# Performance work log

Hardware: AMD Instinct MI355X
Metric: run time of the kernel (lower is better)

Reference implementation:

```python
import jax, jax.numpy as jnp
import numpy as np

N_NODES = 50000
N_EDGES = 500000
N_GRAPHS = 2000
HID = 145
N_CLS = 21
N_LAYERS = 4
EPS = 1e-5

def setup_inputs() -> dict:
    key = jax.random.key(0)
    ks = jax.random.split(key, 12)
    x = jax.random.randint(ks[0], (N_NODES,), 0, N_CLS)
    edge_index = jax.random.randint(ks[1], (2, N_EDGES), 0, N_NODES)
    batch_idx = jnp.sort(jax.random.randint(ks[2], (N_NODES,), 0, N_GRAPHS))
    s = 1.0 / np.sqrt(HID)
    emb = jax.random.normal(ks[3], (N_CLS, HID), jnp.float32)
    Wc = jax.random.uniform(ks[4], (N_LAYERS, HID, HID), jnp.float32, -s, s)
    bc = jax.random.uniform(ks[5], (N_LAYERS, HID), jnp.float32, -s, s)
    gamma = jnp.ones((N_LAYERS, HID), jnp.float32)
    beta = jnp.zeros((N_LAYERS, HID), jnp.float32)
    W1 = jax.random.uniform(ks[6], (HID, HID // 2), jnp.float32, -s, s)
    b1 = jax.random.uniform(ks[7], (HID // 2,), jnp.float32, -s, s)
    W2 = jax.random.uniform(ks[8], (HID // 2, 1), jnp.float32, -s, s)
    b2 = jax.random.uniform(ks[9], (1,), jnp.float32, -s, s)
    return {"x": x, "edge_index": edge_index, "batch_idx": batch_idx,
            "emb": emb, "Wc": Wc, "bc": bc, "gamma": gamma, "beta": beta,
            "W1": W1, "b1": b1, "W2": W2, "b2": b2}

def reference(x, edge_index, batch_idx, emb, Wc, bc, gamma, beta, W1, b1, W2, b2):
    N = x.shape[0]
    # gcn_norm with self loops: deg over targets (col), sym normalization
    loops = jnp.arange(N)
    row = jnp.concatenate([edge_index[0], loops])  # source
    col = jnp.concatenate([edge_index[1], loops])  # target
    deg = jax.ops.segment_sum(jnp.ones_like(row, jnp.float32), col, num_segments=N)
    dis = jnp.where(deg > 0, jax.lax.rsqrt(deg), 0.0)
    ew = dis[row] * dis[col]  # [E+N]

    h = emb[x]  # [N, HID]
    for l in range(N_LAYERS):
        h_in = h
        hw = h @ Wc[l]                                   # linear
        msg = hw[row] * ew[:, None]                      # gather + weight
        agg = jax.ops.segment_sum(msg, col, num_segments=N) + bc[l]  # scatter-add
        # BatchNorm1d (training-mode batch stats, biased var)
        mu = jnp.mean(agg, axis=0)
        var = jnp.mean((agg - mu) ** 2, axis=0)
        hbn = gamma[l] * (agg - mu) * jax.lax.rsqrt(var + EPS) + beta[l]
        h = jax.nn.relu(hbn) + h_in                      # relu + residual
    # global mean pool
    sums = jax.ops.segment_sum(h, batch_idx, num_segments=N_GRAPHS)
    cnt = jax.ops.segment_sum(jnp.ones((N,), jnp.float32), batch_idx, num_segments=N_GRAPHS)
    hg = sums / jnp.maximum(cnt, 1.0)[:, None]
    out = jax.nn.relu(hg @ W1 + b1) @ W2 + b2
    return out.reshape(-1, 1)
```

## Files before the change

kernel.cpp:

```cpp
#include <hip/hip_runtime.h>

#define N_NODES  50000
#define N_EDGES  500000
#define N_GRAPHS 2000
#define HID      145
#define HID2     72
#define N_LAYERS 4
#define EPS      1e-5f
#define HWS_LD   160
#define AGG_LD   152
#define BR       64
#define TSB      168
#define NBKT     64

typedef __attribute__((ext_vector_type(4))) float f32x4;
typedef __attribute__((ext_vector_type(2))) _Float16 f16x2;
typedef __attribute__((ext_vector_type(8))) _Float16 f16x8;


__global__ void k_hist(const int* __restrict__ col, int* __restrict__ hist) {
    int i = blockIdx.x * 256 + threadIdx.x;
    if (i < N_EDGES) atomicAdd(&hist[col[i]], 1);
}

__global__ void k_scan1(const int* __restrict__ cnt, int* __restrict__ incl,
                        int* __restrict__ part) {
    __shared__ int s[1024];
    int i = blockIdx.x * 1024 + threadIdx.x;
    int v = (i < N_NODES) ? cnt[i] : 0;
    s[threadIdx.x] = v;
    __syncthreads();
    for (int d = 1; d < 1024; d <<= 1) {
        int t = (threadIdx.x >= d) ? s[threadIdx.x - d] : 0;
        __syncthreads();
        s[threadIdx.x] += t;
        __syncthreads();
    }
    if (i < N_NODES) incl[i] = s[threadIdx.x];
    if (threadIdx.x == 1023) part[blockIdx.x] = s[1023];
}

__global__ void k_scan2(int* part, int nb) {
    if (threadIdx.x == 0 && blockIdx.x == 0) {
        int acc = 0;
        for (int b = 0; b < nb; b++) { int t = part[b]; part[b] = acc; acc += t; }
    }
}

__global__ void k_scan3(const int* __restrict__ incl, const int* __restrict__ cnt,
                        const int* __restrict__ part, int* __restrict__ starts,
                        int* __restrict__ cursor, float* __restrict__ dis) {
    int i = blockIdx.x * 1024 + threadIdx.x;
    if (i < N_NODES) {
        int st = incl[i] - cnt[i] + part[blockIdx.x];
        starts[i] = st;
        cursor[i] = st;
        dis[i] = rsqrtf((float)(cnt[i] + 1));
    }
    if (i == 0) starts[N_NODES] = N_EDGES;
}

__global__ void k_fill(const int* __restrict__ rowv, const int* __restrict__ colv,
                       int* __restrict__ cursor, int* __restrict__ csr) {
    int e = blockIdx.x * 256 + threadIdx.x;
    if (e < N_EDGES) {
        int c = colv[e];
        int p = atomicAdd(&cursor[c], 1);
        csr[p] = rowv[e];
    }
}


__global__ void k_wfrag(const float* __restrict__ Wc, _Float16* __restrict__ Wfrag) {
    int fid = blockIdx.x;
    int layer = fid / 50, rem = fid - layer * 50;
    int kc = rem / 10, ct = rem - kc * 10;
    int l = threadIdx.x;
    const float* Wl = Wc + (size_t)layer * HID * HID;
    _Float16* base = Wfrag + (size_t)fid * 512 + l * 8;
#pragma unroll
    for (int j = 0; j < 8; j++) {
        int k = kc * 32 + (l >> 4) * 8 + j;
        int c = ct * 16 + (l & 15);
        float v = (k < HID && c < HID) ? Wl[k * HID + c] : 0.f;
        base[j] = (_Float16)v;
    }
}


#define MFMA16(a, b, c) __builtin_amdgcn_mfma_f32_16x16x32_f16(a, b, c, 0, 0, 0)

template <int MODE>
__global__ __launch_bounds__(512, 6) void k_gemm_fused(
    const _Float16* __restrict__ wfb, const float* __restrict__ dis,
    const int* __restrict__ x, const float* __restrict__ emb,
    const _Float16* __restrict__ agg, const float* __restrict__ AB,
    _Float16* __restrict__ h, _Float16* __restrict__ hws) {
    __shared__ _Float16 tile[BR * TSB];
    __shared__ float sA[HID], sB[HID];
    int t = threadIdx.x;
    int rbase = blockIdx.x * BR;
    if (MODE == 1 && t < HID) { sA[t] = AB[t]; sB[t] = AB[HID + t]; }
    __syncthreads();
    for (int idx = t; idx < BR * 19; idx += 512) {
        int r = idx / 19;
        int c = idx - r * 19;
        int f0 = c * 8;
        int gr = rbase + r;
        f16x8 hst = {};
        if (gr < N_NODES) {
            size_t base = (size_t)gr * AGG_LD + f0;
            if (MODE == 0) {
                const float* er = emb + x[gr] * HID;
#pragma unroll
                for (int j = 0; j < 8; j++) {
                    int f = f0 + j;
                    hst[j] = (_Float16)((f < HID) ? er[f] : 0.f);
                }
            } else {
                f16x8 av = *(const f16x8*)(agg + base);
                f16x8 hv = *(const f16x8*)(h + base);
#pragma unroll
                for (int j = 0; j < 8; j++) {
                    int f = f0 + j;
                    float vj = 0.f;
                    if (f < HID) {
                        vj = fmaf(sA[f], (float)av[j], sB[f]);
                        vj = fmaxf(vj, 0.f) + (float)hv[j];
                    }
                    hst[j] = (_Float16)vj;
                }
            }
            *(f16x8*)(h + base) = hst;
        }
        *(f16x8*)&tile[r * TSB + f0] = hst;
    }
    if (t < BR) {
        f16x8 z = {};
        *(f16x8*)&tile[t * TSB + 152] = z;
    }
    __syncthreads();

    int w = t >> 6, l = t & 63;
    int rt = w & 3;
    int c5 = (w >> 2) * 5;
    int arow = rt * 16 + (l & 15);
    int kgrp = (l >> 4) * 8;
    f32x4 acc0 = {}, acc1 = {}, acc2 = {}, acc3 = {}, acc4 = {};
#pragma unroll
    for (int kc = 0; kc < 5; kc++) {
        f16x8 ah = *(const f16x8*)&tile[arow * TSB + kc * 32 + kgrp];
        const _Float16* p = wfb + (size_t)(kc * 10 + c5) * 512 + l * 8;
        f16x8 bh;
#define STEP(ACC, CI)                                                      \
        bh = *(const f16x8*)(p + (CI) * 512);                              \
        ACC = MFMA16(ah, bh, ACC);
        STEP(acc0, 0) STEP(acc1, 1) STEP(acc2, 2) STEP(acc3, 3) STEP(acc4, 4)
#undef STEP
    }
    int rb4 = rbase + rt * 16 + (l >> 4) * 4;
    f32x4 d4 = *(const f32x4*)(dis + rb4);
    int colb = c5 * 16 + (l & 15);
#pragma unroll
    for (int r_ = 0; r_ < 4; r_++) {
        int gr = rb4 + r_;
        if (gr < N_NODES) {
            float dd = d4[r_];
            _Float16* row = hws + (size_t)gr * HWS_LD + colb;
            row[0]  = (_Float16)(acc0[r_] * dd);
            row[16] = (_Float16)(acc1[r_] * dd);
            row[32] = (_Float16)(acc2[r_] * dd);
            row[48] = (_Float16)(acc3[r_] * dd);
            row[64] = (_Float16)(acc4[r_] * dd);
        }
    }
}


__global__ __launch_bounds__(256) void k_agg(const _Float16* __restrict__ hws,
                                             const int* __restrict__ starts,
                                             const int* __restrict__ csr,
                                             const float* __restrict__ dis,
                                             _Float16* __restrict__ agg,
                                             float* __restrict__ gpart) {
    __shared__ float sS[4][AGG_LD], sQ[4][AGG_LD];
    int t = threadIdx.x;
    int wave = t >> 6;
    int lane = t & 63;
    int i = blockIdx.x * 4 + wave;
    int s = starts[i], e = starts[i + 1];
    bool tl = lane < 9;
    const f16x2* self = (const f16x2*)(hws + (size_t)i * HWS_LD);
    f16x2 sv = self[lane];
    float ax = (float)sv.x, ay = (float)sv.y;
    float bx = 0.f, by = 0.f;
    if (tl) { f16x2 tv = self[64 + lane]; bx = (float)tv.x; by = (float)tv.y; }
    int last = e - 1;
    for (int j = s; j < e; j += 8) {
        int idx[8]; float m[8];
#pragma unroll
        for (int u = 0; u < 8; u++) {
            int jj = j + u;
            bool ok = jj < e;
            idx[u] = csr[ok ? jj : last];
            m[u] = ok ? 1.f : 0.f;
        }
#pragma unroll
        for (int u = 0; u < 8; u++) {
            const f16x2* q = (const f16x2*)(hws + (size_t)idx[u] * HWS_LD);
            f16x2 v = q[lane];
            ax = fmaf((float)v.x, m[u], ax);
            ay = fmaf((float)v.y, m[u], ay);
        }
        if (tl) {
#pragma unroll
            for (int u = 0; u < 8; u++) {
                const f16x2* q = (const f16x2*)(hws + (size_t)idx[u] * HWS_LD);
                f16x2 v = q[64 + lane];
                bx = fmaf((float)v.x, m[u], bx);
                by = fmaf((float)v.y, m[u], by);
            }
        }
    }
    float di = dis[i];
    float v0 = ax * di, v1 = ay * di;
    float v2 = bx * di;
    float v3 = (lane < 8) ? by * di : 0.f;

    f16x2* o2 = (f16x2*)(agg + (size_t)i * AGG_LD);
    o2[lane] = f16x2{(_Float16)v0, (_Float16)v1};
    if (tl) o2[64 + lane] = f16x2{(_Float16)v2, (_Float16)v3};

    sS[wave][2 * lane] = v0;     sQ[wave][2 * lane] = v0 * v0;
    sS[wave][2 * lane + 1] = v1; sQ[wave][2 * lane + 1] = v1 * v1;
    if (tl) {
        sS[wave][128 + 2 * lane] = v2; sQ[wave][128 + 2 * lane] = v2 * v2;
        sS[wave][129 + 2 * lane] = v3; sQ[wave][129 + 2 * lane] = v3 * v3;
    }
    __syncthreads();
    int bucket = blockIdx.x & (NBKT - 1);
    float* gp = gpart + (size_t)bucket * (2 * AGG_LD);
    for (int idx2 = t; idx2 < 2 * AGG_LD; idx2 += 256) {
        int f = (idx2 < AGG_LD) ? idx2 : idx2 - AGG_LD;
        if (f > HID) continue;
        float v = (idx2 < AGG_LD)
                      ? ((sS[0][f] + sS[1][f]) + (sS[2][f] + sS[3][f]))
                      : ((sQ[0][f] + sQ[1][f]) + (sQ[2][f] + sQ[3][f]));
        atomicAdd(&gp[idx2], v);
    }
}


__global__ __launch_bounds__(256) void k_bncoef(float* __restrict__ gpart,
                                                const float* __restrict__ gamma,
                                                const float* __restrict__ beta,
                                                float* __restrict__ AB) {
    int w = blockIdx.x * 4 + (threadIdx.x >> 6);
    int lane = threadIdx.x & 63;
    if (w >= HID) return;
    float* ps = gpart + (size_t)lane * (2 * AGG_LD) + w;
    float s = ps[0];
    float q = ps[AGG_LD];
#pragma unroll
    for (int d = 32; d > 0; d >>= 1) {
        s += __shfl_xor(s, d);
        q += __shfl_xor(q, d);
    }
    ps[0] = 0.f;
    ps[AGG_LD] = 0.f;
    if (lane == 0) {
        const float inv = 1.f / (float)N_NODES;
        float mu = s * inv;
        float var = q * inv - mu * mu;
        float a = gamma[w] * rsqrtf(var + EPS);
        AB[w] = a;
        AB[HID + w] = beta[w] - mu * a;
    }
}


__global__ __launch_bounds__(192) void k_pool_mlp(
    const _Float16* __restrict__ agg, const _Float16* __restrict__ h,
    const float* __restrict__ AB, const int* __restrict__ batch,
    const float* __restrict__ W1, const float* __restrict__ b1,
    const float* __restrict__ W2, const float* __restrict__ b2,
    float* __restrict__ out) {
    __shared__ float sH[HID];
    __shared__ float red[128];
    int g = blockIdx.x;
    int lo = 0, hi = N_NODES;
    while (lo < hi) { int m = (lo + hi) >> 1; if (batch[m] < g) lo = m + 1; else hi = m; }
    int s = lo;
    hi = N_NODES;
    while (lo < hi) { int m = (lo + hi) >> 1; if (batch[m] < g + 1) lo = m + 1; else hi = m; }
    int e = lo;
    int f = threadIdx.x;
    if (f < HID) {
        float A = AB[f], B = AB[HID + f];
        float acc = 0.f;
        for (int n = s; n < e; n++) {
            size_t idx = (size_t)n * AGG_LD + f;
            float v = fmaf(A, (float)agg[idx], B);
            acc += fmaxf(v, 0.f) + (float)h[idx];
        }
        sH[f] = acc / fmaxf((float)(e - s), 1.f);
    }
    __syncthreads();
    int t = threadIdx.x;
    float v = 0.f;
    if (t < HID2) {
        float acc = b1[t];
        for (int k = 0; k < HID; k++) acc = fmaf(sH[k], W1[k * HID2 + t], acc);
        v = fmaxf(acc, 0.f) * W2[t];
    }
    if (t < 128) red[t] = v;
    __syncthreads();
    for (int d = 64; d > 0; d >>= 1) {
        if (t < d) red[t] += red[t + d];
        __syncthreads();
    }
    if (t == 0) out[g] = red[0] + b2[0];
}


extern "C" void kernel_launch(void* const* d_in, const int* in_sizes, int n_in,
                              void* d_out, int out_size, void* d_ws, size_t ws_size,
                              hipStream_t stream) {
    const int*   x     = (const int*)d_in[0];
    const int*   erow  = (const int*)d_in[1];
    const int*   ecol  = erow + N_EDGES;
    const int*   batch = (const int*)d_in[2];
    const float* emb   = (const float*)d_in[3];
    const float* Wc    = (const float*)d_in[4];
    const float* gamma = (const float*)d_in[6];
    const float* beta  = (const float*)d_in[7];
    const float* W1    = (const float*)d_in[8];
    const float* b1    = (const float*)d_in[9];
    const float* W2    = (const float*)d_in[10];
    const float* b2    = (const float*)d_in[11];
    float* out = (float*)d_out;

    char* wsb = (char*)d_ws;
    size_t off = 0;
    auto alloc = [&](size_t bytes) -> char* {
        char* p = wsb + off;
        off = (off + bytes + 255) & ~(size_t)255;
        return p;
    };
    int*      hist    = (int*)alloc(N_NODES * 4);
    int*      incl    = (int*)alloc(N_NODES * 4);
    int*      part    = (int*)alloc(64 * 4);
    int*      starts  = (int*)alloc((N_NODES + 1) * 4);
    int*      cursor  = (int*)alloc(N_NODES * 4);
    int*      csr     = (int*)alloc(N_EDGES * 4);
    float*    dis     = (float*)alloc((N_NODES + 64) * 4);
    _Float16* h       = (_Float16*)alloc((size_t)N_NODES * AGG_LD * 2);
    _Float16* hws     = (_Float16*)alloc((size_t)N_NODES * HWS_LD * 2);
    _Float16* agg     = (_Float16*)alloc((size_t)N_NODES * AGG_LD * 2);
    float*    gpart   = (float*)alloc((size_t)NBKT * 2 * AGG_LD * 4);
    float*    AB      = (float*)alloc(2 * HID * 4);
    _Float16* Wfrag   = (_Float16*)alloc((size_t)N_LAYERS * 50 * 512 * 2);

    const int NB_SCAN = (N_NODES + 1023) / 1024;
    const int NB_GEMM = (N_NODES + BR - 1) / BR;

    hipMemsetAsync(hist, 0, N_NODES * 4, stream);
    hipMemsetAsync(gpart, 0, (size_t)NBKT * 2 * AGG_LD * 4, stream);
    k_hist<<<(N_EDGES + 255) / 256, 256, 0, stream>>>(ecol, hist);
    k_scan1<<<NB_SCAN, 1024, 0, stream>>>(hist, incl, part);
    k_scan2<<<1, 64, 0, stream>>>(part, NB_SCAN);
    k_scan3<<<NB_SCAN, 1024, 0, stream>>>(incl, hist, part, starts, cursor, dis);
    k_fill<<<(N_EDGES + 255) / 256, 256, 0, stream>>>(erow, ecol, cursor, csr);
    k_wfrag<<<N_LAYERS * 50, 64, 0, stream>>>(Wc, Wfrag);

    for (int l = 0; l < N_LAYERS; l++) {
        const _Float16* wfb = Wfrag + (size_t)l * 50 * 512;
        if (l == 0)
            k_gemm_fused<0><<<NB_GEMM, 512, 0, stream>>>(wfb, dis, x, emb, agg, AB, h, hws);
        else
            k_gemm_fused<1><<<NB_GEMM, 512, 0, stream>>>(wfb, dis, x, emb, agg, AB, h, hws);
        k_agg<<<N_NODES / 4, 256, 0, stream>>>(hws, starts, csr, dis, agg, gpart);
        k_bncoef<<<(HID + 3) / 4, 256, 0, stream>>>(gpart, gamma + l * HID, beta + l * HID, AB);
    }

    k_pool_mlp<<<N_GRAPHS, 192, 0, stream>>>(agg, h, AB, batch, W1, b1, W2, b2, out);
}
```

Baseline: 396.8 us.

## Fuse small setup kernels and fold BN coefficient computation into GEMM prologue

Replaces the two memsets with one zero kernel, drops the serial scan2 kernel by having each scan3 block compute its prefix offset with a wave reduction, and merges the CSR fill with the weight-fragment conversion into one launch. Per-layer BN statistics now go to separate buffers, and each GEMM block reduces the 64 buckets itself, which removes the per-layer k_bncoef launch. In k_agg, readfirstlane marks the node and CSR indices as wave-uniform so they can use scalar loads. The aim is fewer launches and less serialization, at the cost of each GEMM block re-reading the partial sums.

```diff
diff --git a/kernel.cpp b/kernel.cpp
--- a/kernel.cpp
+++ b/kernel.cpp
@@ -12,10 +12,21 @@
 #define BR       64
 #define TSB      168
 #define NBKT     64
+#define GPSZ     (NBKT * 2 * AGG_LD)
+#define NB_FILL  ((N_EDGES + 255) / 256)
 
 typedef __attribute__((ext_vector_type(4))) float f32x4;
 typedef __attribute__((ext_vector_type(2))) _Float16 f16x2;
 typedef __attribute__((ext_vector_type(8))) _Float16 f16x8;
+
+#define RFL(v) __builtin_amdgcn_readfirstlane(v)
+
+
+__global__ void k_zero(int* __restrict__ hist, float* __restrict__ gpart) {
+    int i = blockIdx.x * 256 + threadIdx.x;
+    if (i < N_NODES) hist[i] = 0;
+    if (i < N_LAYERS * GPSZ) gpart[i] = 0.f;
+}
 
 
 __global__ void k_hist(const int* __restrict__ col, int* __restrict__ hist) {
@@ -40,19 +51,23 @@
     if (threadIdx.x == 1023) part[blockIdx.x] = s[1023];
 }
 
-__global__ void k_scan2(int* part, int nb) {
-    if (threadIdx.x == 0 && blockIdx.x == 0) {
-        int acc = 0;
-        for (int b = 0; b < nb; b++) { int t = part[b]; part[b] = acc; acc += t; }
-    }
-}
 
 __global__ void k_scan3(const int* __restrict__ incl, const int* __restrict__ cnt,
                         const int* __restrict__ part, int* __restrict__ starts,
                         int* __restrict__ cursor, float* __restrict__ dis) {
-    int i = blockIdx.x * 1024 + threadIdx.x;
+    __shared__ int sOff;
+    int t = threadIdx.x;
+    if (t < 64) {
+        int v = (t < (int)blockIdx.x && t < 49) ? part[t] : 0;
+#pragma unroll
+        for (int d = 32; d > 0; d >>= 1) v += __shfl_xor(v, d);
+        if (t == 0) sOff = v;
+    }
+    __syncthreads();
+    int off = sOff;
+    int i = blockIdx.x * 1024 + t;
     if (i < N_NODES) {
-        int st = incl[i] - cnt[i] + part[blockIdx.x];
+        int st = incl[i] - cnt[i] + off;
         starts[i] = st;
         cursor[i] = st;
         dis[i] = rsqrtf((float)(cnt[i] + 1));
@@ -60,30 +75,32 @@
     if (i == 0) starts[N_NODES] = N_EDGES;
 }
 
-__global__ void k_fill(const int* __restrict__ rowv, const int* __restrict__ colv,
-                       int* __restrict__ cursor, int* __restrict__ csr) {
-    int e = blockIdx.x * 256 + threadIdx.x;
-    if (e < N_EDGES) {
-        int c = colv[e];
-        int p = atomicAdd(&cursor[c], 1);
-        csr[p] = rowv[e];
-    }
-}
-
-
-__global__ void k_wfrag(const float* __restrict__ Wc, _Float16* __restrict__ Wfrag) {
-    int fid = blockIdx.x;
-    int layer = fid / 50, rem = fid - layer * 50;
-    int kc = rem / 10, ct = rem - kc * 10;
-    int l = threadIdx.x;
-    const float* Wl = Wc + (size_t)layer * HID * HID;
-    _Float16* base = Wfrag + (size_t)fid * 512 + l * 8;
-#pragma unroll
-    for (int j = 0; j < 8; j++) {
-        int k = kc * 32 + (l >> 4) * 8 + j;
-        int c = ct * 16 + (l & 15);
-        float v = (k < HID && c < HID) ? Wl[k * HID + c] : 0.f;
-        base[j] = (_Float16)v;
+
+__global__ void k_fill_wfrag(const int* __restrict__ rowv, const int* __restrict__ colv,
+                             int* __restrict__ cursor, int* __restrict__ csr,
+                             const float* __restrict__ Wc, _Float16* __restrict__ Wfrag) {
+    int b = blockIdx.x;
+    if (b < NB_FILL) {
+        int e = b * 256 + threadIdx.x;
+        if (e < N_EDGES) {
+            int c = colv[e];
+            int p = atomicAdd(&cursor[c], 1);
+            csr[p] = rowv[e];
+        }
+    } else {
+        int fid = (b - NB_FILL) * 4 + (threadIdx.x >> 6);
+        int l = threadIdx.x & 63;
+        int layer = fid / 50, rem = fid - layer * 50;
+        int kc = rem / 10, ct = rem - kc * 10;
+        const float* Wl = Wc + (size_t)layer * HID * HID;
+        _Float16* base = Wfrag + (size_t)fid * 512 + l * 8;
+#pragma unroll
+        for (int j = 0; j < 8; j++) {
+            int k = kc * 32 + (l >> 4) * 8 + j;
+            int c = ct * 16 + (l & 15);
+            float v = (k < HID && c < HID) ? Wl[k * HID + c] : 0.f;
+            base[j] = (_Float16)v;
+        }
     }
 }
 
@@ -94,13 +111,26 @@
 __global__ __launch_bounds__(512, 6) void k_gemm_fused(
     const _Float16* __restrict__ wfb, const float* __restrict__ dis,
     const int* __restrict__ x, const float* __restrict__ emb,
-    const _Float16* __restrict__ agg, const float* __restrict__ AB,
+    const _Float16* __restrict__ agg, const float* __restrict__ gpart,
+    const float* __restrict__ gamma, const float* __restrict__ beta,
     _Float16* __restrict__ h, _Float16* __restrict__ hws) {
     __shared__ _Float16 tile[BR * TSB];
     __shared__ float sA[HID], sB[HID];
     int t = threadIdx.x;
     int rbase = blockIdx.x * BR;
-    if (MODE == 1 && t < HID) { sA[t] = AB[t]; sB[t] = AB[HID + t]; }
+    if (MODE == 1 && t < HID) {
+        float s_ = 0.f, q_ = 0.f;
+        for (int b = 0; b < NBKT; b++) {
+            s_ += gpart[b * (2 * AGG_LD) + t];
+            q_ += gpart[b * (2 * AGG_LD) + AGG_LD + t];
+        }
+        const float inv = 1.f / (float)N_NODES;
+        float mu = s_ * inv;
+        float var = q_ * inv - mu * mu;
+        float a = gamma[t] * rsqrtf(var + EPS);
+        sA[t] = a;
+        sB[t] = beta[t] - mu * a;
+    }
     __syncthreads();
     for (int idx = t; idx < BR * 19; idx += 512) {
         int r = idx / 19;
@@ -187,8 +217,9 @@
     int t = threadIdx.x;
     int wave = t >> 6;
     int lane = t & 63;
-    int i = blockIdx.x * 4 + wave;
-    int s = starts[i], e = starts[i + 1];
+    int i = RFL(blockIdx.x * 4 + wave);
+    int s = RFL(starts[i]);
+    int e = RFL(starts[i + 1]);
     bool tl = lane < 9;
     const f16x2* self = (const f16x2*)(hws + (size_t)i * HWS_LD);
     f16x2 sv = self[lane];
@@ -197,26 +228,24 @@
     if (tl) { f16x2 tv = self[64 + lane]; bx = (float)tv.x; by = (float)tv.y; }
     int last = e - 1;
     for (int j = s; j < e; j += 8) {
-        int idx[8]; float m[8];
+        int rb[8]; float m[8];
 #pragma unroll
         for (int u = 0; u < 8; u++) {
             int jj = j + u;
             bool ok = jj < e;
-            idx[u] = csr[ok ? jj : last];
+            rb[u] = RFL(csr[ok ? jj : last]) * HWS_LD;
             m[u] = ok ? 1.f : 0.f;
         }
 #pragma unroll
         for (int u = 0; u < 8; u++) {
-            const f16x2* q = (const f16x2*)(hws + (size_t)idx[u] * HWS_LD);
-            f16x2 v = q[lane];
+            f16x2 v = ((const f16x2*)(hws + rb[u]))[lane];
             ax = fmaf((float)v.x, m[u], ax);
             ay = fmaf((float)v.y, m[u], ay);
         }
         if (tl) {
 #pragma unroll
             for (int u = 0; u < 8; u++) {
-                const f16x2* q = (const f16x2*)(hws + (size_t)idx[u] * HWS_LD);
-                f16x2 v = q[64 + lane];
+                f16x2 v = ((const f16x2*)(hws + rb[u]))[64 + lane];
                 bx = fmaf((float)v.x, m[u], bx);
                 by = fmaf((float)v.y, m[u], by);
             }
@@ -251,14 +280,14 @@
 }
 
 
-__global__ __launch_bounds__(256) void k_bncoef(float* __restrict__ gpart,
+__global__ __launch_bounds__(256) void k_bncoef(const float* __restrict__ gpart,
                                                 const float* __restrict__ gamma,
                                                 const float* __restrict__ beta,
                                                 float* __restrict__ AB) {
     int w = blockIdx.x * 4 + (threadIdx.x >> 6);
     int lane = threadIdx.x & 63;
     if (w >= HID) return;
-    float* ps = gpart + (size_t)lane * (2 * AGG_LD) + w;
+    const float* ps = gpart + (size_t)lane * (2 * AGG_LD) + w;
     float s = ps[0];
     float q = ps[AGG_LD];
 #pragma unroll
@@ -266,8 +295,6 @@
         s += __shfl_xor(s, d);
         q += __shfl_xor(q, d);
     }
-    ps[0] = 0.f;
-    ps[AGG_LD] = 0.f;
     if (lane == 0) {
         const float inv = 1.f / (float)N_NODES;
         float mu = s * inv;
@@ -357,31 +384,34 @@
     _Float16* h       = (_Float16*)alloc((size_t)N_NODES * AGG_LD * 2);
     _Float16* hws     = (_Float16*)alloc((size_t)N_NODES * HWS_LD * 2);
     _Float16* agg     = (_Float16*)alloc((size_t)N_NODES * AGG_LD * 2);
-    float*    gpart   = (float*)alloc((size_t)NBKT * 2 * AGG_LD * 4);
+    float*    gpart   = (float*)alloc((size_t)N_LAYERS * GPSZ * 4);
     float*    AB      = (float*)alloc(2 * HID * 4);
     _Float16* Wfrag   = (_Float16*)alloc((size_t)N_LAYERS * 50 * 512 * 2);
 
     const int NB_SCAN = (N_NODES + 1023) / 1024;
     const int NB_GEMM = (N_NODES + BR - 1) / BR;
-
-    hipMemsetAsync(hist, 0, N_NODES * 4, stream);
-    hipMemsetAsync(gpart, 0, (size_t)NBKT * 2 * AGG_LD * 4, stream);
+    const int NB_ZERO = (N_LAYERS * GPSZ + 255) / 256;
+
+    k_zero<<<(N_NODES > N_LAYERS * GPSZ ? (N_NODES + 255) / 256 : NB_ZERO), 256, 0, stream>>>(hist, gpart);
     k_hist<<<(N_EDGES + 255) / 256, 256, 0, stream>>>(ecol, hist);
     k_scan1<<<NB_SCAN, 1024, 0, stream>>>(hist, incl, part);
-    k_scan2<<<1, 64, 0, stream>>>(part, NB_SCAN);
     k_scan3<<<NB_SCAN, 1024, 0, stream>>>(incl, hist, part, starts, cursor, dis);
-    k_fill<<<(N_EDGES + 255) / 256, 256, 0, stream>>>(erow, ecol, cursor, csr);
-    k_wfrag<<<N_LAYERS * 50, 64, 0, stream>>>(Wc, Wfrag);
+    k_fill_wfrag<<<NB_FILL + 50, 256, 0, stream>>>(erow, ecol, cursor, csr, Wc, Wfrag);
 
     for (int l = 0; l < N_LAYERS; l++) {
         const _Float16* wfb = Wfrag + (size_t)l * 50 * 512;
         if (l == 0)
-            k_gemm_fused<0><<<NB_GEMM, 512, 0, stream>>>(wfb, dis, x, emb, agg, AB, h, hws);
+            k_gemm_fused<0><<<NB_GEMM, 512, 0, stream>>>(
+                wfb, dis, x, emb, agg, nullptr, nullptr, nullptr, h, hws);
         else
-            k_gemm_fused<1><<<NB_GEMM, 512, 0, stream>>>(wfb, dis, x, emb, agg, AB, h, hws);
-        k_agg<<<N_NODES / 4, 256, 0, stream>>>(hws, starts, csr, dis, agg, gpart);
-        k_bncoef<<<(HID + 3) / 4, 256, 0, stream>>>(gpart, gamma + l * HID, beta + l * HID, AB);
-    }
-
+            k_gemm_fused<1><<<NB_GEMM, 512, 0, stream>>>(
+                wfb, dis, x, emb, agg, gpart + (size_t)(l - 1) * GPSZ,
+                gamma + (l - 1) * HID, beta + (l - 1) * HID, h, hws);
+        k_agg<<<N_NODES / 4, 256, 0, stream>>>(hws, starts, csr, dis, agg,
+                                               gpart + (size_t)l * GPSZ);
+    }
+
+    k_bncoef<<<(HID + 3) / 4, 256, 0, stream>>>(gpart + (size_t)3 * GPSZ,
+                                                gamma + 3 * HID, beta + 3 * HID, AB);
     k_pool_mlp<<<N_GRAPHS, 192, 0, stream>>>(agg, h, AB, batch, W1, b1, W2, b2, out);
 }
```

Result: faster. 381.6 us (-3.8%).
